# Kernel tuning notes

Measured on AMD Instinct MI355X. Metric: run time of the kernel, lower is better.

Reference implementation:

```python
import jax, jax.numpy as jnp
import numpy as np

TOP_K = 2  # num_experts_per_tok

def setup_inputs() -> dict:
    key = jax.random.key(0)
    ks = jax.random.split(key, 6)
    B, S, D, E, H = 4, 2048, 1024, 8, 4096
    x  = jax.random.normal(ks[0], (B, S, D), dtype=jnp.float32)
    Wg = jax.random.normal(ks[1], (D, E), dtype=jnp.float32) * 0.02
    W1 = jax.random.normal(ks[2], (E, D, H), dtype=jnp.float32) * 0.02
    b1 = jnp.zeros((E, H), dtype=jnp.float32)
    W2 = jax.random.normal(ks[3], (E, H, D), dtype=jnp.float32) * 0.02
    b2 = jnp.zeros((E, D), dtype=jnp.float32)
    return {"x": x, "Wg": Wg, "W1": W1, "b1": b1, "W2": W2, "b2": b2}

def reference(x, Wg, W1, b1, W2, b2):
    B, S, D = x.shape
    E = Wg.shape[1]
    xf = x.reshape(-1, D)                       # [T, D]
    T = xf.shape[0]
    logits = xf @ Wg                            # [T, E]
    probs = jax.nn.softmax(logits, axis=-1)
    weights, indices = jax.lax.top_k(probs, TOP_K)   # [T, K]
    # Dense combine weights: cw[t, e] = routing weight if e in top-k of t else 0.
    cw = jnp.zeros((T, E), dtype=x.dtype).at[jnp.arange(T)[:, None], indices].set(weights)
    out = jnp.zeros_like(xf)
    for e in range(E):  # small fixed expert count; per-expert GEMMs
        h = jax.nn.gelu(xf @ W1[e] + b1[e], approximate=False)  # [T, H]
        y = h @ W2[e] + b2[e]                                   # [T, D]
        out = out + y * cw[:, e:e + 1]
    return out.reshape(B, S, D)
```

## Files before the change

### kernel.cpp

```cpp
#include <hip/hip_runtime.h>
#include <hip/hip_bf16.h>
#include <stdint.h>

#define D_DIM 1024
#define E_NUM 8
#define H_DIM 4096

typedef __attribute__((ext_vector_type(8))) short short8;
typedef __attribute__((ext_vector_type(4))) short short4v;
typedef __attribute__((ext_vector_type(4))) unsigned short ushort4v;
typedef __attribute__((ext_vector_type(4))) float f32x4;

#define GLOBAL_AS __attribute__((address_space(1)))
#define LDS_AS __attribute__((address_space(3)))

__device__ __forceinline__ void async_load16(const void* g, void* l) {
    __builtin_amdgcn_global_load_lds((GLOBAL_AS void*)g, (LDS_AS void*)l, 16, 0, 0);
}

__device__ __forceinline__ float gelu_fast(float x) {
    float x3 = x * x * x;
    float z = 0.7978845608028654f * x + 0.0356774081363001f * x3;
    float u = __expf(-2.0f * fabsf(z));
    float t = __fdividef(1.0f - u, 1.0f + u);
    t = copysignf(t, z);
    return 0.5f * x * (1.0f + t);
}

__device__ __forceinline__ float b2f(short s) {
    union { float f; unsigned u; } x; x.u = ((unsigned)(unsigned short)s) << 16; return x.f;
}

__device__ __forceinline__ unsigned short f2b(float f) {
    union { __hip_bfloat16 h; unsigned short s; } u;
    u.h = __float2bfloat16(f);
    return u.s;
}

__global__ __launch_bounds__(256) void router_kernel(
    const float* __restrict__ x, const float* __restrict__ Wg,
    __hip_bfloat16* __restrict__ xb, int* __restrict__ cnt,
    int* __restrict__ tok, int* __restrict__ eidx, float* __restrict__ ewgt, int T) {
    int gwave = (int)((blockIdx.x * 256 + threadIdx.x) >> 6);
    int lane = threadIdx.x & 63;
    if (gwave >= T) return;
    const float* xr = x + (size_t)gwave * D_DIM;
    double acc[E_NUM];
#pragma unroll
    for (int e = 0; e < E_NUM; ++e) acc[e] = 0.0;
#pragma unroll
    for (int i = 0; i < D_DIM / 64; ++i) {
        int d = i * 64 + lane;
        float xv = xr[d];
        xb[(size_t)gwave * D_DIM + d] = __float2bfloat16(xv);
        const float4* wgp = (const float4*)(Wg + (size_t)d * E_NUM);
        float4 wa = wgp[0], wb = wgp[1];
        double xd = (double)xv;
        acc[0] += xd * (double)wa.x; acc[1] += xd * (double)wa.y;
        acc[2] += xd * (double)wa.z; acc[3] += xd * (double)wa.w;
        acc[4] += xd * (double)wb.x; acc[5] += xd * (double)wb.y;
        acc[6] += xd * (double)wb.z; acc[7] += xd * (double)wb.w;
    }
#pragma unroll
    for (int s = 32; s > 0; s >>= 1) {
#pragma unroll
        for (int e = 0; e < E_NUM; ++e) acc[e] += __shfl_xor(acc[e], s);
    }
    double mx = acc[0];
#pragma unroll
    for (int e = 1; e < E_NUM; ++e) mx = fmax(mx, acc[e]);
    double p[E_NUM]; double sum = 0.0;
#pragma unroll
    for (int e = 0; e < E_NUM; ++e) { p[e] = exp(acc[e] - mx); sum += p[e]; }
    int i0 = 0;
#pragma unroll
    for (int e = 1; e < E_NUM; ++e) if (p[e] > p[i0]) i0 = e;
    int i1 = (i0 == 0) ? 1 : 0;
#pragma unroll
    for (int e = 0; e < E_NUM; ++e) if (e != i0 && p[e] > p[i1]) i1 = e;
    float w0 = (float)(p[i0] / sum);
    float w1 = (float)(p[i1] / sum);
    if (lane == 0) {
        int s0 = atomicAdd(&cnt[i0], 1);
        tok[i0 * T + s0] = gwave;
        eidx[2 * gwave]     = (i0 << 16) | s0;
        ewgt[2 * gwave]     = w0;
        int s1 = atomicAdd(&cnt[i1], 1);
        tok[i1 * T + s1] = gwave;
        eidx[2 * gwave + 1] = (i1 << 16) | s1;
        ewgt[2 * gwave + 1] = w1;
    }
}

__global__ void prefix_kernel(const int* __restrict__ cnt, int* __restrict__ base) {
    if (threadIdx.x == 0) {
        int a = 0;
#pragma unroll
        for (int e = 0; e < E_NUM; ++e) { base[e] = a; a += cnt[e]; }
    }
}

__global__ __launch_bounds__(256) void transpose_conv_kernel(
    const float* __restrict__ in, __hip_bfloat16* __restrict__ out, int R, int C) {
    __shared__ float tile[32][33];
    int e = blockIdx.z;
    int c0 = blockIdx.x * 32, r0 = blockIdx.y * 32;
    const float* ip = in + (size_t)e * R * C;
    __hip_bfloat16* op = out + (size_t)e * C * R;
    int tx = threadIdx.x, ty = threadIdx.y;
#pragma unroll
    for (int i = 0; i < 32; i += 8)
        tile[ty + i][tx] = ip[(size_t)(r0 + ty + i) * C + (c0 + tx)];
    __syncthreads();
#pragma unroll
    for (int i = 0; i < 32; i += 8)
        op[(size_t)(c0 + ty + i) * R + (r0 + tx)] = __float2bfloat16(tile[tx][ty + i]);
}

__global__ __launch_bounds__(256) void transpose_w2_kernel(
    const float* __restrict__ in, __hip_bfloat16* __restrict__ out) {
    __shared__ float tile[64][33];
    int e = blockIdx.z;
    int d0 = blockIdx.x * 32, h0 = blockIdx.y * 64;
    const float* ip = in + (size_t)e * H_DIM * D_DIM;
    unsigned short* op = (unsigned short*)(out + (size_t)e * D_DIM * H_DIM);
    int tx = threadIdx.x, ty = threadIdx.y;
#pragma unroll
    for (int i = 0; i < 64; i += 8) {
        int j = ty + i;
        int src = (j & 3) * 16 + (j >> 2);
        tile[j][tx] = ip[(size_t)(h0 + src) * D_DIM + (d0 + tx)];
    }
    __syncthreads();
#pragma unroll
    for (int i = 0; i < 32; i += 8) {
        int d = ty + i;
        unsigned pk = (unsigned)f2b(tile[2 * tx][d]) | ((unsigned)f2b(tile[2 * tx + 1][d]) << 16);
        *(unsigned*)(op + (size_t)(d0 + d) * H_DIM + h0 + 2 * tx) = pk;
    }
}


__global__ __launch_bounds__(256) void gemm1_kernel(
    const __hip_bfloat16* __restrict__ xb,
    const __hip_bfloat16* __restrict__ w1t,
    const float* __restrict__ b1,
    const int* __restrict__ cnt, const int* __restrict__ base,
    const int* __restrict__ tok,
    __hip_bfloat16* __restrict__ hbuf,
    int T) {
    int e = blockIdx.z;
    int M = cnt[e];
    int m0 = blockIdx.y * 128;
    if (m0 >= M) return;
    int n0 = blockIdx.x * 128;
    const __hip_bfloat16* Bp = w1t + (size_t)e * H_DIM * D_DIM;

    __shared__ __align__(16) short sA[128 * 32];
    __shared__ __align__(16) short sB[128 * 32];
    __shared__ float sBias[128];
    char* sAc = (char*)sA; char* sBc = (char*)sB;

    int tid = threadIdx.x;
    int w = tid >> 6, lane = tid & 63;
    int wm = w >> 1, wn = w & 1;
    int q = lane >> 4, l4 = lane & 15;

    if (tid < 128) sBias[tid] = b1[e * H_DIM + n0 + tid];

    int kswz = ((lane & 3) ^ ((lane >> 3) & 3)) << 3;
    int r0 = w * 32 + (lane >> 2);
    int r1 = r0 + 16;
    int tA0 = tok[e * T + min(m0 + r0, M - 1)];
    int tA1 = tok[e * T + min(m0 + r1, M - 1)];
    const __hip_bfloat16* gA0 = xb + (size_t)tA0 * D_DIM + kswz;
    const __hip_bfloat16* gA1 = xb + (size_t)tA1 * D_DIM + kswz;
    const __hip_bfloat16* gB0 = Bp + (size_t)(n0 + r0) * D_DIM + kswz;
    const __hip_bfloat16* gB1 = Bp + (size_t)(n0 + r1) * D_DIM + kswz;
    char* lA0 = sAc + w * 2048; char* lA1 = lA0 + 1024;
    char* lB0 = sBc + w * 2048; char* lB1 = lB0 + 1024;

    f32x4 acc[4][4];
#pragma unroll
    for (int a = 0; a < 4; ++a)
#pragma unroll
        for (int b = 0; b < 4; ++b) acc[a][b] = (f32x4){0.f, 0.f, 0.f, 0.f};

    for (int kk = 0; kk < D_DIM; kk += 32) {
        async_load16(gA0 + kk, lA0);
        async_load16(gA1 + kk, lA1);
        async_load16(gB0 + kk, lB0);
        async_load16(gB1 + kk, lB1);
        __syncthreads();
        short8 aF[4], bF[4];
#pragma unroll
        for (int t = 0; t < 4; ++t) {
            int ra = wm * 64 + t * 16 + l4;
            aF[t] = *(const short8*)(sAc + ra * 64 + ((q ^ ((ra >> 1) & 3)) << 4));
            int rb = wn * 64 + t * 16 + l4;
            bF[t] = *(const short8*)(sBc + rb * 64 + ((q ^ ((rb >> 1) & 3)) << 4));
        }
#pragma unroll
        for (int tm = 0; tm < 4; ++tm)
#pragma unroll
            for (int tn = 0; tn < 4; ++tn)
                acc[tm][tn] = __builtin_amdgcn_mfma_f32_16x16x32_bf16(aF[tm], bF[tn], acc[tm][tn], 0, 0, 0);
        __syncthreads();
    }

    int sb = base[e];
    unsigned short* hs = (unsigned short*)hbuf;
#pragma unroll
    for (int tm = 0; tm < 4; ++tm) {
        int rbase = wm * 64 + tm * 16 + q * 4;
#pragma unroll
        for (int i = 0; i < 4; ++i) {
            int row = m0 + rbase + i;
            if (row < M) {
                size_t hrow = (size_t)(sb + row) * H_DIM;
                ushort4v pk;
#pragma unroll
                for (int tn = 0; tn < 4; ++tn) {
                    float v = acc[tm][tn][i] + sBias[wn * 64 + tn * 16 + l4];
                    pk[tn] = f2b(gelu_fast(v));
                }
                *(ushort4v*)(hs + hrow + n0 + wn * 64 + l4 * 4) = pk;
            }
        }
    }
}

__global__ __launch_bounds__(256) void gemm2_kernel(
    const __hip_bfloat16* __restrict__ hbuf,
    const __hip_bfloat16* __restrict__ w2t,
    const int* __restrict__ cnt, const int* __restrict__ base,
    __hip_bfloat16* __restrict__ ybuf,
    int T) {
    int e = blockIdx.z >> 1;
    int kc = blockIdx.z & 1;
    int M = cnt[e];
    int m0 = blockIdx.y * 128;
    if (m0 >= M) return;
    int n0 = blockIdx.x * 128;
    int sb = base[e];
    const __hip_bfloat16* Bp = w2t + (size_t)e * D_DIM * H_DIM;

    __shared__ __align__(16) short sA[128 * 32];
    __shared__ __align__(16) short sB[128 * 32];
    char* sAc = (char*)sA; char* sBc = (char*)sB;

    int tid = threadIdx.x;
    int w = tid >> 6, lane = tid & 63;
    int wm = w >> 1, wn = w & 1;
    int q = lane >> 4, l4 = lane & 15;

    int kswz = ((lane & 3) ^ ((lane >> 3) & 3)) << 3;
    int r0 = w * 32 + (lane >> 2);
    int r1 = r0 + 16;
    const __hip_bfloat16* gA0 = hbuf + (size_t)(sb + min(m0 + r0, M - 1)) * H_DIM + kswz;
    const __hip_bfloat16* gA1 = hbuf + (size_t)(sb + min(m0 + r1, M - 1)) * H_DIM + kswz;
    const __hip_bfloat16* gB0 = Bp + (size_t)(n0 + r0) * H_DIM + kswz;
    const __hip_bfloat16* gB1 = Bp + (size_t)(n0 + r1) * H_DIM + kswz;
    char* lA0 = sAc + w * 2048; char* lA1 = lA0 + 1024;
    char* lB0 = sBc + w * 2048; char* lB1 = lB0 + 1024;

    f32x4 acc[4][4];
#pragma unroll
    for (int a = 0; a < 4; ++a)
#pragma unroll
        for (int b = 0; b < 4; ++b) acc[a][b] = (f32x4){0.f, 0.f, 0.f, 0.f};

    int k0 = kc * (H_DIM / 2), k1 = k0 + (H_DIM / 2);
    for (int kk = k0; kk < k1; kk += 32) {
        async_load16(gA0 + kk, lA0);
        async_load16(gA1 + kk, lA1);
        async_load16(gB0 + kk, lB0);
        async_load16(gB1 + kk, lB1);
        __syncthreads();
        short8 aF[4], bF[4];
#pragma unroll
        for (int t = 0; t < 4; ++t) {
            int ra = wm * 64 + t * 16 + l4;
            aF[t] = *(const short8*)(sAc + ra * 64 + ((q ^ ((ra >> 1) & 3)) << 4));
            int rb = wn * 64 + t * 16 + l4;
            bF[t] = *(const short8*)(sBc + rb * 64 + ((q ^ ((rb >> 1) & 3)) << 4));
        }
#pragma unroll
        for (int tm = 0; tm < 4; ++tm)
#pragma unroll
            for (int tn = 0; tn < 4; ++tn)
                acc[tm][tn] = __builtin_amdgcn_mfma_f32_16x16x32_bf16(aF[tm], bF[tn], acc[tm][tn], 0, 0, 0);
        __syncthreads();
    }

    size_t ybase = (size_t)kc * 2 * T;
    unsigned short* ys = (unsigned short*)ybuf;
#pragma unroll
    for (int tm = 0; tm < 4; ++tm) {
        int rbase = wm * 64 + tm * 16 + q * 4;
#pragma unroll
        for (int i = 0; i < 4; ++i) {
            int row = m0 + rbase + i;
            if (row < M) {
                size_t yrow = (ybase + sb + row) * D_DIM;
                ushort4v pk;
#pragma unroll
                for (int tn = 0; tn < 4; ++tn) pk[tn] = f2b(acc[tm][tn][i]);
                *(ushort4v*)(ys + yrow + n0 + wn * 64 + l4 * 4) = pk;
            }
        }
    }
}

__global__ __launch_bounds__(256) void combine_kernel(
    const __hip_bfloat16* __restrict__ yb, const float* __restrict__ b2,
    const int* __restrict__ base, const int* __restrict__ eidx,
    const float* __restrict__ ewgt, float* __restrict__ out, int T) {
    int t = blockIdx.x, tid = threadIdx.x;
    int v0 = eidx[2 * t], v1 = eidx[2 * t + 1];
    float w0 = ewgt[2 * t], w1 = ewgt[2 * t + 1];
    int e0 = v0 >> 16, e1 = v1 >> 16;
    size_t g0 = (size_t)base[e0] + (v0 & 0xffff);
    size_t g1 = (size_t)base[e1] + (v1 & 0xffff);
    int c = tid * 4;
    int blk = c >> 6;
    int tt = (c >> 2) & 15;
    size_t off2 = (size_t)2 * T * D_DIM;
    const short* ys = (const short*)yb;
    short4v a0 = *(const short4v*)(ys + g0 * D_DIM + c);
    short4v a1 = *(const short4v*)(ys + off2 + g0 * D_DIM + c);
    short4v c0 = *(const short4v*)(ys + g1 * D_DIM + c);
    short4v c1 = *(const short4v*)(ys + off2 + g1 * D_DIM + c);
    float s0[4] = { b2f(a0.x) + b2f(a1.x), b2f(a0.y) + b2f(a1.y),
                    b2f(a0.z) + b2f(a1.z), b2f(a0.w) + b2f(a1.w) };
    float s1[4] = { b2f(c0.x) + b2f(c1.x), b2f(c0.y) + b2f(c1.y),
                    b2f(c0.z) + b2f(c1.z), b2f(c0.w) + b2f(c1.w) };
    float* orow = out + (size_t)t * D_DIM;
#pragma unroll
    for (int s = 0; s < 4; ++s) {
        int oc = blk * 64 + s * 16 + tt;
        float o = w0 * (s0[s] + b2[(size_t)e0 * D_DIM + oc]) +
                  w1 * (s1[s] + b2[(size_t)e1 * D_DIM + oc]);
        orow[oc] = o;
    }
}

extern "C" void kernel_launch(void* const* d_in, const int* in_sizes, int n_in,
                              void* d_out, int out_size, void* d_ws, size_t ws_size,
                              hipStream_t stream) {
    const float* x  = (const float*)d_in[0];
    const float* Wg = (const float*)d_in[1];
    const float* W1 = (const float*)d_in[2];
    const float* b1 = (const float*)d_in[3];
    const float* W2 = (const float*)d_in[4];
    const float* b2 = (const float*)d_in[5];
    int T = in_sizes[0] / D_DIM;

    char* p = (char*)d_ws;
    int* cnt   = (int*)p;
    int* base  = (int*)(p + 256);
    int* tok   = (int*)(p + 512);
    int* eidx  = (int*)(p + 512 + 4ll * E_NUM * T);
    float* ewgt = (float*)(p + 512 + 4ll * E_NUM * T + 8ll * T);
    char* pb = p + 512 + 4ll * E_NUM * T + 16ll * T;
    __hip_bfloat16* xb  = (__hip_bfloat16*)pb;
    __hip_bfloat16* w1t = xb + (size_t)T * D_DIM;
    __hip_bfloat16* w2t = w1t + (size_t)E_NUM * H_DIM * D_DIM;
    __hip_bfloat16* hb  = w2t + (size_t)E_NUM * H_DIM * D_DIM;
    __hip_bfloat16* yb  = xb;

    hipMemsetAsync(cnt, 0, 256, stream);

    router_kernel<<<dim3((T + 3) / 4), 256, 0, stream>>>(x, Wg, xb, cnt, tok, eidx, ewgt, T);
    prefix_kernel<<<1, 64, 0, stream>>>(cnt, base);
    transpose_conv_kernel<<<dim3(H_DIM / 32, D_DIM / 32, E_NUM), dim3(32, 8), 0, stream>>>(W1, w1t, D_DIM, H_DIM);
    transpose_w2_kernel<<<dim3(D_DIM / 32, H_DIM / 64, E_NUM), dim3(32, 8), 0, stream>>>(W2, w2t);
    gemm1_kernel<<<dim3(H_DIM / 128, T / 128, E_NUM), 256, 0, stream>>>(xb, w1t, b1, cnt, base, tok, hb, T);
    gemm2_kernel<<<dim3(D_DIM / 128, T / 128, E_NUM * 2), 256, 0, stream>>>(hb, w2t, cnt, base, yb, T);
    combine_kernel<<<T, 256, 0, stream>>>(yb, b2, base, eidx, ewgt, (float*)d_out, T);
}
```

Before: 906.5 us.

## Double GEMM K-tile, merge weight transposes, and batch router atomics per block

Both expert GEMMs now stage a 64-wide K slice per iteration instead of 32, with a new 8-way XOR swizzle. This halves the number of barrier pairs per K sweep at the cost of doubled LDS per block. The two weight transpose/convert kernels are merged into one launch that uses 64x64 tiles and float2 loads. Routing is split so the router only records expert picks, and a new bucket kernel assigns slots using shared-memory counters plus one global atomic per expert per block, replacing per-token global atomics.

```diff
diff --git a/kernel.cpp b/kernel.cpp
--- a/kernel.cpp
+++ b/kernel.cpp
@@ -39,8 +39,8 @@
 
 __global__ __launch_bounds__(256) void router_kernel(
     const float* __restrict__ x, const float* __restrict__ Wg,
-    __hip_bfloat16* __restrict__ xb, int* __restrict__ cnt,
-    int* __restrict__ tok, int* __restrict__ eidx, float* __restrict__ ewgt, int T) {
+    __hip_bfloat16* __restrict__ xb, int* __restrict__ epick,
+    float* __restrict__ ewgt, int T) {
     int gwave = (int)((blockIdx.x * 256 + threadIdx.x) >> 6);
     int lane = threadIdx.x & 63;
     if (gwave >= T) return;
@@ -78,18 +78,31 @@
     int i1 = (i0 == 0) ? 1 : 0;
 #pragma unroll
     for (int e = 0; e < E_NUM; ++e) if (e != i0 && p[e] > p[i1]) i1 = e;
-    float w0 = (float)(p[i0] / sum);
-    float w1 = (float)(p[i1] / sum);
     if (lane == 0) {
-        int s0 = atomicAdd(&cnt[i0], 1);
-        tok[i0 * T + s0] = gwave;
-        eidx[2 * gwave]     = (i0 << 16) | s0;
-        ewgt[2 * gwave]     = w0;
-        int s1 = atomicAdd(&cnt[i1], 1);
-        tok[i1 * T + s1] = gwave;
-        eidx[2 * gwave + 1] = (i1 << 16) | s1;
-        ewgt[2 * gwave + 1] = w1;
-    }
+        epick[gwave] = i0 | (i1 << 8);
+        ewgt[2 * gwave]     = (float)(p[i0] / sum);
+        ewgt[2 * gwave + 1] = (float)(p[i1] / sum);
+    }
+}
+
+__global__ __launch_bounds__(256) void bucket_kernel(
+    const int* __restrict__ epick, int* __restrict__ cnt,
+    int* __restrict__ tok, int* __restrict__ eidx, int T) {
+    __shared__ int lcnt[E_NUM];
+    __shared__ int gbase[E_NUM];
+    int b = blockIdx.x, tid = threadIdx.x;
+    if (tid < E_NUM) lcnt[tid] = 0;
+    __syncthreads();
+    int t = b * 128 + (tid >> 1);
+    int j = tid & 1;
+    int e = (epick[t] >> (j * 8)) & 0xff;
+    int li = atomicAdd(&lcnt[e], 1);
+    __syncthreads();
+    if (tid < E_NUM) gbase[tid] = atomicAdd(&cnt[tid], lcnt[tid]);
+    __syncthreads();
+    int slot = gbase[e] + li;
+    tok[e * T + slot] = t;
+    eidx[2 * t + j] = (e << 16) | slot;
 }
 
 __global__ void prefix_kernel(const int* __restrict__ cnt, int* __restrict__ base) {
@@ -100,43 +113,41 @@
     }
 }
 
-__global__ __launch_bounds__(256) void transpose_conv_kernel(
-    const float* __restrict__ in, __hip_bfloat16* __restrict__ out, int R, int C) {
-    __shared__ float tile[32][33];
+__global__ __launch_bounds__(256) void transpose_both_kernel(
+    const float* __restrict__ W1, const float* __restrict__ W2,
+    __hip_bfloat16* __restrict__ w1t, __hip_bfloat16* __restrict__ w2t) {
+    __shared__ float tile[64][65];
     int e = blockIdx.z;
-    int c0 = blockIdx.x * 32, r0 = blockIdx.y * 32;
-    const float* ip = in + (size_t)e * R * C;
-    __hip_bfloat16* op = out + (size_t)e * C * R;
+    int id = blockIdx.x;
+    const float* src; unsigned short* dst; int R, C, r0, c0, perm;
+    if (id < 1024) {
+        R = D_DIM; C = H_DIM;
+        r0 = (id >> 6) * 64; c0 = (id & 63) * 64;
+        src = W1 + (size_t)e * D_DIM * H_DIM;
+        dst = (unsigned short*)(w1t + (size_t)e * H_DIM * D_DIM);
+        perm = 0;
+    } else {
+        id -= 1024;
+        R = H_DIM; C = D_DIM;
+        r0 = (id >> 4) * 64; c0 = (id & 15) * 64;
+        src = W2 + (size_t)e * H_DIM * D_DIM;
+        dst = (unsigned short*)(w2t + (size_t)e * D_DIM * H_DIM);
+        perm = 1;
+    }
     int tx = threadIdx.x, ty = threadIdx.y;
 #pragma unroll
-    for (int i = 0; i < 32; i += 8)
-        tile[ty + i][tx] = ip[(size_t)(r0 + ty + i) * C + (c0 + tx)];
+    for (int i = 0; i < 8; ++i) {
+        int j = ty + i * 8;
+        int sr = perm ? ((j & 3) * 16 + (j >> 2)) : j;
+        float2 v = *(const float2*)(src + (size_t)(r0 + sr) * C + c0 + 2 * tx);
+        tile[j][2 * tx] = v.x; tile[j][2 * tx + 1] = v.y;
+    }
     __syncthreads();
 #pragma unroll
-    for (int i = 0; i < 32; i += 8)
-        op[(size_t)(c0 + ty + i) * R + (r0 + tx)] = __float2bfloat16(tile[tx][ty + i]);
-}
-
-__global__ __launch_bounds__(256) void transpose_w2_kernel(
-    const float* __restrict__ in, __hip_bfloat16* __restrict__ out) {
-    __shared__ float tile[64][33];
-    int e = blockIdx.z;
-    int d0 = blockIdx.x * 32, h0 = blockIdx.y * 64;
-    const float* ip = in + (size_t)e * H_DIM * D_DIM;
-    unsigned short* op = (unsigned short*)(out + (size_t)e * D_DIM * H_DIM);
-    int tx = threadIdx.x, ty = threadIdx.y;
-#pragma unroll
-    for (int i = 0; i < 64; i += 8) {
-        int j = ty + i;
-        int src = (j & 3) * 16 + (j >> 2);
-        tile[j][tx] = ip[(size_t)(h0 + src) * D_DIM + (d0 + tx)];
-    }
-    __syncthreads();
-#pragma unroll
-    for (int i = 0; i < 32; i += 8) {
-        int d = ty + i;
-        unsigned pk = (unsigned)f2b(tile[2 * tx][d]) | ((unsigned)f2b(tile[2 * tx + 1][d]) << 16);
-        *(unsigned*)(op + (size_t)(d0 + d) * H_DIM + h0 + 2 * tx) = pk;
+    for (int i = 0; i < 8; ++i) {
+        int cc = ty + i * 8;
+        unsigned pk = (unsigned)f2b(tile[2 * tx][cc]) | ((unsigned)f2b(tile[2 * tx + 1][cc]) << 16);
+        *(unsigned*)(dst + (size_t)(c0 + cc) * R + r0 + 2 * tx) = pk;
     }
 }
 
@@ -156,8 +167,8 @@
     int n0 = blockIdx.x * 128;
     const __hip_bfloat16* Bp = w1t + (size_t)e * H_DIM * D_DIM;
 
-    __shared__ __align__(16) short sA[128 * 32];
-    __shared__ __align__(16) short sB[128 * 32];
+    __shared__ __align__(16) short sA[128 * 64];
+    __shared__ __align__(16) short sB[128 * 64];
     __shared__ float sBias[128];
     char* sAc = (char*)sA; char* sBc = (char*)sB;
 
@@ -168,17 +179,18 @@
 
     if (tid < 128) sBias[tid] = b1[e * H_DIM + n0 + tid];
 
-    int kswz = ((lane & 3) ^ ((lane >> 3) & 3)) << 3;
-    int r0 = w * 32 + (lane >> 2);
-    int r1 = r0 + 16;
-    int tA0 = tok[e * T + min(m0 + r0, M - 1)];
-    int tA1 = tok[e * T + min(m0 + r1, M - 1)];
-    const __hip_bfloat16* gA0 = xb + (size_t)tA0 * D_DIM + kswz;
-    const __hip_bfloat16* gA1 = xb + (size_t)tA1 * D_DIM + kswz;
-    const __hip_bfloat16* gB0 = Bp + (size_t)(n0 + r0) * D_DIM + kswz;
-    const __hip_bfloat16* gB1 = Bp + (size_t)(n0 + r1) * D_DIM + kswz;
-    char* lA0 = sAc + w * 2048; char* lA1 = lA0 + 1024;
-    char* lB0 = sBc + w * 2048; char* lB1 = lB0 + 1024;
+    int rl = lane >> 3;
+    int g = (lane & 7) ^ rl;
+    const __hip_bfloat16* gA[4]; const __hip_bfloat16* gB[4];
+#pragma unroll
+    for (int i = 0; i < 4; ++i) {
+        int r = w * 32 + i * 8 + rl;
+        int tA = tok[e * T + min(m0 + r, M - 1)];
+        gA[i] = xb + (size_t)tA * D_DIM + g * 8;
+        gB[i] = Bp + (size_t)(n0 + r) * D_DIM + g * 8;
+    }
+    char* lA = sAc + w * 4096 + lane * 16;
+    char* lB = sBc + w * 4096 + lane * 16;
 
     f32x4 acc[4][4];
 #pragma unroll
@@ -186,25 +198,29 @@
 #pragma unroll
         for (int b = 0; b < 4; ++b) acc[a][b] = (f32x4){0.f, 0.f, 0.f, 0.f};
 
-    for (int kk = 0; kk < D_DIM; kk += 32) {
-        async_load16(gA0 + kk, lA0);
-        async_load16(gA1 + kk, lA1);
-        async_load16(gB0 + kk, lB0);
-        async_load16(gB1 + kk, lB1);
+    for (int kk = 0; kk < D_DIM; kk += 64) {
+#pragma unroll
+        for (int i = 0; i < 4; ++i) async_load16(gA[i] + kk, lA + i * 1024);
+#pragma unroll
+        for (int i = 0; i < 4; ++i) async_load16(gB[i] + kk, lB + i * 1024);
         __syncthreads();
-        short8 aF[4], bF[4];
-#pragma unroll
-        for (int t = 0; t < 4; ++t) {
-            int ra = wm * 64 + t * 16 + l4;
-            aF[t] = *(const short8*)(sAc + ra * 64 + ((q ^ ((ra >> 1) & 3)) << 4));
-            int rb = wn * 64 + t * 16 + l4;
-            bF[t] = *(const short8*)(sBc + rb * 64 + ((q ^ ((rb >> 1) & 3)) << 4));
+#pragma unroll
+        for (int s = 0; s < 2; ++s) {
+            short8 aF[4], bF[4];
+            int cg = s * 4 + q;
+#pragma unroll
+            for (int t = 0; t < 4; ++t) {
+                int ra = wm * 64 + t * 16 + l4;
+                aF[t] = *(const short8*)(sAc + ra * 128 + ((cg ^ (ra & 7)) << 4));
+                int rb = wn * 64 + t * 16 + l4;
+                bF[t] = *(const short8*)(sBc + rb * 128 + ((cg ^ (rb & 7)) << 4));
+            }
+#pragma unroll
+            for (int tm = 0; tm < 4; ++tm)
+#pragma unroll
+                for (int tn = 0; tn < 4; ++tn)
+                    acc[tm][tn] = __builtin_amdgcn_mfma_f32_16x16x32_bf16(aF[tm], bF[tn], acc[tm][tn], 0, 0, 0);
         }
-#pragma unroll
-        for (int tm = 0; tm < 4; ++tm)
-#pragma unroll
-            for (int tn = 0; tn < 4; ++tn)
-                acc[tm][tn] = __builtin_amdgcn_mfma_f32_16x16x32_bf16(aF[tm], bF[tn], acc[tm][tn], 0, 0, 0);
         __syncthreads();
     }
 
@@ -245,8 +261,8 @@
     int sb = base[e];
     const __hip_bfloat16* Bp = w2t + (size_t)e * D_DIM * H_DIM;
 
-    __shared__ __align__(16) short sA[128 * 32];
-    __shared__ __align__(16) short sB[128 * 32];
+    __shared__ __align__(16) short sA[128 * 64];
+    __shared__ __align__(16) short sB[128 * 64];
     char* sAc = (char*)sA; char* sBc = (char*)sB;
 
     int tid = threadIdx.x;
@@ -254,15 +270,17 @@
     int wm = w >> 1, wn = w & 1;
     int q = lane >> 4, l4 = lane & 15;
 
-    int kswz = ((lane & 3) ^ ((lane >> 3) & 3)) << 3;
-    int r0 = w * 32 + (lane >> 2);
-    int r1 = r0 + 16;
-    const __hip_bfloat16* gA0 = hbuf + (size_t)(sb + min(m0 + r0, M - 1)) * H_DIM + kswz;
-    const __hip_bfloat16* gA1 = hbuf + (size_t)(sb + min(m0 + r1, M - 1)) * H_DIM + kswz;
-    const __hip_bfloat16* gB0 = Bp + (size_t)(n0 + r0) * H_DIM + kswz;
-    const __hip_bfloat16* gB1 = Bp + (size_t)(n0 + r1) * H_DIM + kswz;
-    char* lA0 = sAc + w * 2048; char* lA1 = lA0 + 1024;
-    char* lB0 = sBc + w * 2048; char* lB1 = lB0 + 1024;
+    int rl = lane >> 3;
+    int g = (lane & 7) ^ rl;
+    const __hip_bfloat16* gA[4]; const __hip_bfloat16* gB[4];
+#pragma unroll
+    for (int i = 0; i < 4; ++i) {
+        int r = w * 32 + i * 8 + rl;
+        gA[i] = hbuf + (size_t)(sb + min(m0 + r, M - 1)) * H_DIM + g * 8;
+        gB[i] = Bp + (size_t)(n0 + r) * H_DIM + g * 8;
+    }
+    char* lA = sAc + w * 4096 + lane * 16;
+    char* lB = sBc + w * 4096 + lane * 16;
 
     f32x4 acc[4][4];
 #pragma unroll
@@ -271,25 +289,29 @@
         for (int b = 0; b < 4; ++b) acc[a][b] = (f32x4){0.f, 0.f, 0.f, 0.f};
 
     int k0 = kc * (H_DIM / 2), k1 = k0 + (H_DIM / 2);
-    for (int kk = k0; kk < k1; kk += 32) {
-        async_load16(gA0 + kk, lA0);
-        async_load16(gA1 + kk, lA1);
-        async_load16(gB0 + kk, lB0);
-        async_load16(gB1 + kk, lB1);
+    for (int kk = k0; kk < k1; kk += 64) {
+#pragma unroll
+        for (int i = 0; i < 4; ++i) async_load16(gA[i] + kk, lA + i * 1024);
+#pragma unroll
+        for (int i = 0; i < 4; ++i) async_load16(gB[i] + kk, lB + i * 1024);
         __syncthreads();
-        short8 aF[4], bF[4];
-#pragma unroll
-        for (int t = 0; t < 4; ++t) {
-            int ra = wm * 64 + t * 16 + l4;
-            aF[t] = *(const short8*)(sAc + ra * 64 + ((q ^ ((ra >> 1) & 3)) << 4));
-            int rb = wn * 64 + t * 16 + l4;
-            bF[t] = *(const short8*)(sBc + rb * 64 + ((q ^ ((rb >> 1) & 3)) << 4));
+#pragma unroll
+        for (int s = 0; s < 2; ++s) {
+            short8 aF[4], bF[4];
+            int cg = s * 4 + q;
+#pragma unroll
+            for (int t = 0; t < 4; ++t) {
+                int ra = wm * 64 + t * 16 + l4;
+                aF[t] = *(const short8*)(sAc + ra * 128 + ((cg ^ (ra & 7)) << 4));
+                int rb = wn * 64 + t * 16 + l4;
+                bF[t] = *(const short8*)(sBc + rb * 128 + ((cg ^ (rb & 7)) << 4));
+            }
+#pragma unroll
+            for (int tm = 0; tm < 4; ++tm)
+#pragma unroll
+                for (int tn = 0; tn < 4; ++tn)
+                    acc[tm][tn] = __builtin_amdgcn_mfma_f32_16x16x32_bf16(aF[tm], bF[tn], acc[tm][tn], 0, 0, 0);
         }
-#pragma unroll
-        for (int tm = 0; tm < 4; ++tm)
-#pragma unroll
-            for (int tn = 0; tn < 4; ++tn)
-                acc[tm][tn] = __builtin_amdgcn_mfma_f32_16x16x32_bf16(aF[tm], bF[tn], acc[tm][tn], 0, 0, 0);
         __syncthreads();
     }
 
@@ -362,7 +384,8 @@
     int* tok   = (int*)(p + 512);
     int* eidx  = (int*)(p + 512 + 4ll * E_NUM * T);
     float* ewgt = (float*)(p + 512 + 4ll * E_NUM * T + 8ll * T);
-    char* pb = p + 512 + 4ll * E_NUM * T + 16ll * T;
+    int* epick = (int*)(p + 512 + 4ll * E_NUM * T + 16ll * T);
+    char* pb = p + 512 + 4ll * E_NUM * T + 20ll * T;
     __hip_bfloat16* xb  = (__hip_bfloat16*)pb;
     __hip_bfloat16* w1t = xb + (size_t)T * D_DIM;
     __hip_bfloat16* w2t = w1t + (size_t)E_NUM * H_DIM * D_DIM;
@@ -371,10 +394,10 @@
 
     hipMemsetAsync(cnt, 0, 256, stream);
 
-    router_kernel<<<dim3((T + 3) / 4), 256, 0, stream>>>(x, Wg, xb, cnt, tok, eidx, ewgt, T);
+    router_kernel<<<dim3((T + 3) / 4), 256, 0, stream>>>(x, Wg, xb, epick, ewgt, T);
+    bucket_kernel<<<dim3(T / 128), 256, 0, stream>>>(epick, cnt, tok, eidx, T);
     prefix_kernel<<<1, 64, 0, stream>>>(cnt, base);
-    transpose_conv_kernel<<<dim3(H_DIM / 32, D_DIM / 32, E_NUM), dim3(32, 8), 0, stream>>>(W1, w1t, D_DIM, H_DIM);
-    transpose_w2_kernel<<<dim3(D_DIM / 32, H_DIM / 64, E_NUM), dim3(32, 8), 0, stream>>>(W2, w2t);
+    transpose_both_kernel<<<dim3(2048, 1, E_NUM), dim3(32, 8), 0, stream>>>(W1, W2, w1t, w2t);
     gemm1_kernel<<<dim3(H_DIM / 128, T / 128, E_NUM), 256, 0, stream>>>(xb, w1t, b1, cnt, base, tok, hb, T);
     gemm2_kernel<<<dim3(D_DIM / 128, T / 128, E_NUM * 2), 256, 0, stream>>>(hb, w2t, cnt, base, yb, T);
     combine_kernel<<<T, 256, 0, stream>>>(yb, b2, base, eidx, ewgt, (float*)d_out, T);
```

Result: faster. 825.0 us (-9.0%).
